# Kernel tuning notes

Hardware: AMD Instinct MI355X
Metric: run time of the kernel (lower is better)

The kernel has to match this reference:

```python
import jax, jax.numpy as jnp
import numpy as np

B, C, X, Y, Z = 2, 4, 128, 128, 96
_BIG = 1e10  # effectively infinite squared distance (no background in line)


def _edt_sq_pass(f, axis):
    """One separable pass of the exact squared EDT along `axis`:
    g[i] = min_j f[j] + (i - j)^2  (Felzenszwalb lower envelope, brute-forced
    with lax.map so only O(rest) memory per step)."""
    f = jnp.moveaxis(f, axis, -1)  # (..., L)
    idx = jnp.arange(f.shape[-1], dtype=f.dtype)
    g = jax.lax.map(lambda i: jnp.min(f + (i - idx) ** 2, axis=-1), idx)  # (L, ...)
    return jnp.moveaxis(jnp.moveaxis(g, 0, -1), -1, axis)


def _edt(mask):
    """Exact Euclidean distance of True voxels to the nearest False voxel
    (matches scipy.ndimage.distance_transform_edt on a binary mask)."""
    f = jnp.where(mask, _BIG, 0.0).astype(jnp.float32)
    for ax in (-3, -2, -1):  # three spatial axes
        f = _edt_sq_pass(f, ax)
    return jnp.sqrt(f)


def _neighbor(m, axis, d):
    """Shift `m` by d along `axis` with edge replication (reflect border,
    as in skimage's grey erosion used by find_boundaries)."""
    axis = axis % m.ndim
    pw = [(1, 1) if i == axis else (0, 0) for i in range(m.ndim)]
    p = jnp.pad(m, pw, mode='edge')
    sl = [slice(None)] * m.ndim
    sl[axis] = slice(1 + d, p.shape[axis] - 1 + d)
    return p[tuple(sl)]


def _inner_boundary(m):
    """skimage find_boundaries(mode='inner', connectivity=1): foreground voxels
    with at least one background face-neighbor."""
    eroded = m
    for ax in (-3, -2, -1):
        eroded = eroded & _neighbor(m, ax, 1) & _neighbor(m, ax, -1)
    return m & ~eroded


def _compute_sdf(onehot):
    """Signed distance map per (batch, class): negdis - posdis, zero on the
    inner boundary; zero where the class is absent; channel 0 is skipped."""
    posdis = _edt(onehot)          # dist inside object to background
    negdis = _edt(~onehot)         # dist outside object to foreground
    sdf = jnp.where(_inner_boundary(onehot), 0.0, negdis - posdis)
    any_pos = jnp.any(onehot, axis=(2, 3, 4), keepdims=True)
    sdf = jnp.where(any_pos, sdf, 0.0)
    return sdf.at[:, 0].set(0.0)   # loop starts at c=1 in the original


def setup_inputs() -> dict:
    key = jax.random.key(0)
    k1, k2 = jax.random.split(key)
    net_output = jax.random.normal(k1, (B, C, X, Y, Z), dtype=jnp.float32)
    gt = jax.random.randint(k2, (B, 1, X, Y, Z), 0, C, dtype=jnp.int32)
    return {"net_output": net_output, "gt": gt}


def reference(net_output, gt):
    probs = jax.nn.softmax(net_output, axis=1)  # softmax_helper = softmax over class dim
    classes = jnp.arange(net_output.shape[1], dtype=gt.dtype).reshape(1, -1, 1, 1, 1)
    onehot = gt == classes  # scatter_(1, gt, 1) one-hot, bool (B,C,X,Y,Z)
    phi = _compute_sdf(onehot)
    # einsum('bcxyz,bcxyz->bcxyz') on foreground channels, then global mean
    return jnp.mean(probs[:, 1:] * phi[:, 1:])
```

## Files before the change

kernel.cpp:

```cpp
#include <hip/hip_runtime.h>
#include <hip/hip_fp16.h>
#include <math.h>

#define XD 128
#define YD 128
#define ZD 96
#define NV (XD*YD*ZD)
#define SXX (YD*ZD)
#define SENT 49152
#define TW2 114
#define TDW (TW2/2)
#define TROWS 144
#define SCANB 192
#define PROBB 1024

__global__ __launch_bounds__(384) void k_scan_prob(const int* __restrict__ gt,
                                                   const float* __restrict__ net,
                                                   unsigned char* __restrict__ out,
                                                   __half2* __restrict__ probs,
                                                   int* __restrict__ flags,
                                                   int batch0) {
    const int bb  = blockIdx.y;
    const int myb = batch0 + bb;
    const int tid = threadIdx.x;

    if (blockIdx.x >= SCANB) {
        const int p = (blockIdx.x - SCANB) * 384 + tid;
        const int idx = p * 4;
        const float* nb = net + (size_t)myb * 4 * NV;
        float4 v0 = *(const float4*)(nb + idx);
        float4 v1 = *(const float4*)(nb + NV + idx);
        float4 v2 = *(const float4*)(nb + 2 * NV + idx);
        float4 v3 = *(const float4*)(nb + 3 * NV + idx);

        const float a0[4] = {v0.x, v0.y, v0.z, v0.w};
        const float a1[4] = {v1.x, v1.y, v1.z, v1.w};
        const float a2[4] = {v2.x, v2.y, v2.z, v2.w};
        const float a3[4] = {v3.x, v3.y, v3.z, v3.w};
        float p1[4], p2[4], p3[4];
#pragma unroll
        for (int j = 0; j < 4; ++j) {
            float mx = fmaxf(fmaxf(a0[j], a1[j]), fmaxf(a2[j], a3[j]));
            float e0 = __expf(a0[j] - mx);
            float e1 = __expf(a1[j] - mx);
            float e2 = __expf(a2[j] - mx);
            float e3 = __expf(a3[j] - mx);
            float iv = __frcp_rn(e0 + e1 + e2 + e3);
            p1[j] = e1 * iv; p2[j] = e2 * iv; p3[j] = e3 * iv;
        }
        __half2 h10 = __floats2half2_rn(p1[0], p1[1]);
        __half2 h11 = __floats2half2_rn(p1[2], p1[3]);
        __half2 h20 = __floats2half2_rn(p2[0], p2[1]);
        __half2 h21 = __floats2half2_rn(p2[2], p2[3]);
        __half2 h30 = __floats2half2_rn(p3[0], p3[1]);
        __half2 h31 = __floats2half2_rn(p3[2], p3[3]);
        ((__half2*)probs)[(size_t)(myb * 3 + 0) * (NV / 2) + 2 * p]     = h10;
        ((__half2*)probs)[(size_t)(myb * 3 + 0) * (NV / 2) + 2 * p + 1] = h11;
        ((__half2*)probs)[(size_t)(myb * 3 + 1) * (NV / 2) + 2 * p]     = h20;
        ((__half2*)probs)[(size_t)(myb * 3 + 1) * (NV / 2) + 2 * p + 1] = h21;
        ((__half2*)probs)[(size_t)(myb * 3 + 2) * (NV / 2) + 2 * p]     = h30;
        ((__half2*)probs)[(size_t)(myb * 3 + 2) * (NV / 2) + 2 * p + 1] = h31;
        return;
    }

    const int l   = tid & 63;
    const int w6  = tid >> 6;
    const int lq0 = blockIdx.x * 64;

    __shared__ unsigned char gtile[64 * 132];
    __shared__ int blkbits;
    if (tid == 0) blkbits = 0;

    int mybits = 0;
    const int* gp = gt + (size_t)myb * NV + lq0 + l;
    for (int j = w6; j < XD; j += 6) {
        int g = gp[(size_t)j * SXX];
        mybits |= 1 << g;
        gtile[l * 132 + j] = (unsigned char)g;
    }
#pragma unroll
    for (int off = 32; off; off >>= 1) mybits |= __shfl_xor(mybits, off);
    __syncthreads();
    if ((tid & 63) == 0) atomicOr(&blkbits, mybits);

    unsigned int D[32];
    {
        const unsigned int ci = (unsigned int)((w6 >> 1) + 1);
        const int s = w6 & 1;
        unsigned int G[32];
        const unsigned int* grow = (const unsigned int*)gtile + l * 33;
#pragma unroll
        for (int q = 0; q < 32; ++q) G[q] = grow[q];

        int cnt = 200;
#pragma unroll
        for (int q = 0; q < 32; ++q) {
            unsigned int u = G[q], dv = 0;
#pragma unroll
            for (int b = 0; b < 4; ++b) {
                unsigned int gv = (u >> (8 * b)) & 255u;
                bool zero = s ? (gv == ci) : (gv != ci);
                cnt = zero ? 0 : ((cnt < 200) ? cnt + 1 : 200);
                dv |= (unsigned int)cnt << (8 * b);
            }
            D[q] = dv;
        }
        cnt = 200;
#pragma unroll
        for (int q = 31; q >= 0; --q) {
            unsigned int u = G[q], dv = D[q];
#pragma unroll
            for (int b = 3; b >= 0; --b) {
                unsigned int gv = (u >> (8 * b)) & 255u;
                bool zero = s ? (gv == ci) : (gv != ci);
                cnt = zero ? 0 : ((cnt < 200) ? cnt + 1 : 200);
                unsigned int old = (dv >> (8 * b)) & 255u;
                unsigned int nbv = ((unsigned int)cnt < old) ? (unsigned int)cnt : old;
                dv = (dv & ~(255u << (8 * b))) | (nbv << (8 * b));
            }
            D[q] = dv;
        }
    }
    __syncthreads();
    if (tid == 0) atomicOr(&flags[myb], blkbits);

    {
        const int r = l & 3;
        unsigned char* ob = out + (size_t)(bb * 6 + w6) * NV + lq0 + (l & ~3);
#pragma unroll
        for (int q = 0; q < 32; ++q) {
            unsigned int A = D[q];
            unsigned int Bv = (unsigned int)__shfl_xor((int)A, 1);
            unsigned int t = (r & 1)
                ? __builtin_amdgcn_perm(A, Bv, 0x07030501u)
                : __builtin_amdgcn_perm(A, Bv, 0x02060004u);
            unsigned int Cv = (unsigned int)__shfl_xor((int)t, 2);
            unsigned int y = (r & 2)
                ? __builtin_amdgcn_perm(t, Cv, 0x07060302u)
                : __builtin_amdgcn_perm(t, Cv, 0x01000504u);
            *(unsigned int*)(ob + (size_t)(4 * q + r) * SXX) = y;
        }
    }
}

__device__ __forceinline__ bool edt_fast(const float r[32], float m[16]) {
#pragma unroll
    for (int k = 0; k < 16; ++k) m[k] = r[k + 8];
#pragma unroll
    for (int t = 1; t <= 4; ++t) {
        const float t2 = (float)(t * t);
#pragma unroll
        for (int k = 0; k < 16; ++k)
            m[k] = fminf(m[k], fminf(r[k + 8 - t], r[k + 8 + t]) + t2);
    }
    float mm = m[0];
#pragma unroll
    for (int k = 1; k < 16; ++k) mm = fmaxf(mm, m[k]);
    if (__all(mm <= 16.0f)) return true;
#pragma unroll
    for (int t = 5; t <= 8; ++t) {
        const float t2 = (float)(t * t);
#pragma unroll
        for (int k = 0; k < 16; ++k)
            m[k] = fminf(m[k], fminf(r[k + 8 - t], r[k + 8 + t]) + t2);
    }
    mm = m[0];
#pragma unroll
    for (int k = 1; k < 16; ++k) mm = fmaxf(mm, m[k]);
    return __all(mm <= 64.0f) != 0;
}

template<int STRIDE, int L>
__device__ __forceinline__ void edt_slow(const unsigned short* __restrict__ p0,
                                         int i0, float m[16]) {
    int t = 9;
    bool done = false;
    while (!done && t < L) {
        for (int u = 0; u < 4; ++u, ++t) {
            float t2 = (float)(t * t);
#pragma unroll
            for (int k = 0; k < 16; ++k) {
                int jm = i0 + k - t; if (jm < -8) jm = -8;
                int jp = i0 + k + t; if (jp > L + 7) jp = L + 7;
                m[k] = fminf(m[k], fminf((float)p0[jm * STRIDE],
                                         (float)p0[jp * STRIDE]) + t2);
            }
        }
        float mm = m[0];
#pragma unroll
        for (int k = 1; k < 16; ++k) mm = fmaxf(mm, m[k]);
        done = __all(mm <= (float)((t - 1) * (t - 1))) != 0;
    }
}

__global__ __launch_bounds__(768) void k_yz_acc(const unsigned char* __restrict__ in,
                                                const __half2* __restrict__ probs,
                                                const int* __restrict__ flags,
                                                double* __restrict__ partials,
                                                int batch0) {
    const int x   = blockIdx.x;
    const int bbl = blockIdx.y / 3;
    const int c   = blockIdx.y % 3;
    const int b   = batch0 + bbl;
    const int tid = threadIdx.x;
    const int pidx = (b * 3 + c) * XD + x;

    __shared__ unsigned short tile[TROWS * TW2];
    __shared__ double sd[768];
    unsigned int* t32 = (unsigned int*)tile;

    if (((flags[b] >> (c + 1)) & 1) == 0) {
        if (tid == 0) partials[pidx] = 0.0;
        return;
    }

    for (int i = tid; i < 16 * TDW; i += 768) {
        int r = i / TDW, cc = i - r * TDW;
        int row = (r < 8) ? r : 128 + r;
        t32[row * TDW + cc] = 0xFFFFFFFFu;
    }
    for (int i = tid; i < 128 * 9; i += 768) {
        int r = i / 9, cc = i - r * 9;
        int col = (cc < 4) ? cc : (48 + cc);
        t32[(8 + r) * TDW + col] = 0xFFFFFFFFu;
    }

    const int z0 = tid % 96;  const int iY = (tid / 96) * 16;
    const int y0 = tid % 128; const int iZ = (tid / 128) * 16;
    const int e  = tid * 16;
    const int sy = e / ZD, sz = e - sy * ZD;
    const unsigned int sbase = (8 + sy) * TDW + (8 + sz) / 2;

    float m[16];
    unsigned int dpp[8];

    {
        const uint4* ip = (const uint4*)(in + (size_t)(bbl * 6 + 2 * c) * NV +
                                         (size_t)x * SXX);
        uint4 v = ip[tid];
        unsigned int vv[4] = {v.x, v.y, v.z, v.w};
#pragma unroll
        for (int q = 0; q < 4; ++q) {
            unsigned int b0 = vv[q] & 255u, b1 = (vv[q] >> 8) & 255u;
            unsigned int b2 = (vv[q] >> 16) & 255u, b3 = vv[q] >> 24;
            t32[sbase + 2 * q] = (b0 > 127u ? SENT : b0 * b0) |
                                 ((b1 > 127u ? SENT : b1 * b1) << 16);
            t32[sbase + 2 * q + 1] = (b2 > 127u ? SENT : b2 * b2) |
                                     ((b3 > 127u ? SENT : b3 * b3) << 16);
        }
    }
    __syncthreads();
    {
        float r[32];
#pragma unroll
        for (int w = 0; w < 32; ++w) r[w] = (float)tile[(iY + w) * TW2 + 8 + z0];
        if (!edt_fast(r, m)) edt_slow<TW2, YD>(&tile[8 * TW2 + 8 + z0], iY, m);
        __syncthreads();
#pragma unroll
        for (int k = 0; k < 16; ++k)
            tile[(8 + iY + k) * TW2 + 8 + z0] =
                (unsigned short)fminf(m[k], (float)SENT);
        __syncthreads();
    }
    {
        float r[32];
        const unsigned int* wp = &t32[(8 + y0) * TDW + iZ / 2];
#pragma unroll
        for (int q = 0; q < 16; ++q) {
            unsigned int u = wp[q];
            r[2 * q] = (float)(u & 0xFFFFu);
            r[2 * q + 1] = (float)(u >> 16);
        }
        if (!edt_fast(r, m)) edt_slow<1, ZD>(&tile[(8 + y0) * TW2 + 8], iZ, m);
    }
#pragma unroll
    for (int q = 0; q < 8; ++q)
        dpp[q] = (unsigned int)fminf(m[2 * q], (float)SENT) |
                 ((unsigned int)fminf(m[2 * q + 1], (float)SENT) << 16);
    __syncthreads();

    {
        const uint4* ip = (const uint4*)(in + (size_t)(bbl * 6 + 2 * c + 1) * NV +
                                         (size_t)x * SXX);
        uint4 v = ip[tid];
        unsigned int vv[4] = {v.x, v.y, v.z, v.w};
#pragma unroll
        for (int q = 0; q < 4; ++q) {
            unsigned int b0 = vv[q] & 255u, b1 = (vv[q] >> 8) & 255u;
            unsigned int b2 = (vv[q] >> 16) & 255u, b3 = vv[q] >> 24;
            t32[sbase + 2 * q] = (b0 > 127u ? SENT : b0 * b0) |
                                 ((b1 > 127u ? SENT : b1 * b1) << 16);
            t32[sbase + 2 * q + 1] = (b2 > 127u ? SENT : b2 * b2) |
                                     ((b3 > 127u ? SENT : b3 * b3) << 16);
        }
    }
    __syncthreads();
    {
        float r[32];
#pragma unroll
        for (int w = 0; w < 32; ++w) r[w] = (float)tile[(iY + w) * TW2 + 8 + z0];
        if (!edt_fast(r, m)) edt_slow<TW2, YD>(&tile[8 * TW2 + 8 + z0], iY, m);
        __syncthreads();
#pragma unroll
        for (int k = 0; k < 16; ++k)
            tile[(8 + iY + k) * TW2 + 8 + z0] =
                (unsigned short)fminf(m[k], (float)SENT);
        __syncthreads();
    }
    {
        float r[32];
        const unsigned int* wp = &t32[(8 + y0) * TDW + iZ / 2];
#pragma unroll
        for (int q = 0; q < 16; ++q) {
            unsigned int u = wp[q];
            r[2 * q] = (float)(u & 0xFFFFu);
            r[2 * q + 1] = (float)(u >> 16);
        }
        if (!edt_fast(r, m)) edt_slow<1, ZD>(&tile[(8 + y0) * TW2 + 8], iZ, m);
    }

    float a = 0.0f;
    {
        const __half2* pv = probs + (size_t)(b * 3 + c) * (NV / 2) +
                            ((size_t)x * SXX + (size_t)y0 * ZD + iZ) / 2;
#pragma unroll
        for (int q = 0; q < 8; ++q) {
            float2 pf = __half22float2(pv[q]);
            unsigned int dp0 = dpp[q] & 0xFFFFu, dp1 = dpp[q] >> 16;
            float phi0 = (dp0 == 1u) ? 0.0f
                       : (sqrtf(m[2 * q]) - sqrtf((float)dp0));
            float phi1 = (dp1 == 1u) ? 0.0f
                       : (sqrtf(m[2 * q + 1]) - sqrtf((float)dp1));
            a += pf.x * phi0 + pf.y * phi1;
        }
    }
    sd[tid] = (double)a;
    __syncthreads();
    for (int off = 512; off; off >>= 1) {
        if (tid < off && tid + off < 768) sd[tid] += sd[tid + off];
        __syncthreads();
    }
    if (tid == 0) partials[pidx] = sd[0];
}

__global__ void k_reduce(const double* __restrict__ partials, int n,
                         float* __restrict__ out) {
    __shared__ double sd[256];
    double ls = 0.0;
    for (int i = threadIdx.x; i < n; i += 256) ls += partials[i];
    sd[threadIdx.x] = ls;
    __syncthreads();
    for (int off = 128; off > 0; off >>= 1) {
        if (threadIdx.x < off) sd[threadIdx.x] += sd[threadIdx.x + off];
        __syncthreads();
    }
    if (threadIdx.x == 0) out[0] = (float)(sd[0] / 9437184.0);
}

extern "C" void kernel_launch(void* const* d_in, const int* in_sizes, int n_in,
                              void* d_out, int out_size, void* d_ws, size_t ws_size,
                              hipStream_t stream) {
    const float* net = (const float*)d_in[0];
    const int*   gt  = (const int*)d_in[1];
    float* out = (float*)d_out;
    char* ws = (char*)d_ws;

    const size_t xbufB1  = (size_t)6 * NV;
    const size_t probsB  = (size_t)2 * 3 * NV * 2;
    const size_t tail    = (size_t)768 * sizeof(double) + 64;

    const int nb = (ws_size >= 2 * xbufB1 + probsB + tail) ? 2 : 1;

    unsigned char* xbuf  = (unsigned char*)ws;
    __half2*       probs = (__half2*)(ws + (size_t)nb * xbufB1);
    double*     partials = (double*)(ws + (size_t)nb * xbufB1 + probsB);
    int*           flags = (int*)((char*)partials + 768 * sizeof(double));

    hipMemsetAsync(flags, 0, 8 * sizeof(int), stream);

    for (int b0 = 0; b0 < 2; b0 += nb) {
        hipLaunchKernelGGL(k_scan_prob, dim3(SCANB + PROBB, nb), dim3(384), 0,
                           stream, gt, net, xbuf, probs, flags, b0);
        hipLaunchKernelGGL(k_yz_acc, dim3(XD, 3 * nb), dim3(768), 0, stream,
                           xbuf, probs, flags, partials, b0);
    }
    hipLaunchKernelGGL(k_reduce, dim3(1), dim3(256), 0, stream, partials,
                       768, out);
}
```

Before: 75.35 us.

## Run Y/Z EDT passes with packed u16 min/add instead of float

The Y and Z distance-transform passes in k_yz_acc now keep squared distances as packed 16-bit pairs and use v_pk_min_u16/v_pk_add_u16. This halves the ALU instruction count and register footprint compared with per-element float min/add. The thread mapping changes so that each thread handles 8 packed words, column-pair in Y and a 16-element chunk in Z, with alignbit used for the odd shifts. The rare long-distance fallback still runs in float. Risks are u16 saturation, since values are capped at the 49152 sentinel plus t² up to 64, and the added pack/unpack overhead on the slow path.

```diff
diff --git a/kernel.cpp b/kernel.cpp
--- a/kernel.cpp
+++ b/kernel.cpp
@@ -8,6 +8,7 @@
 #define NV (XD*YD*ZD)
 #define SXX (YD*ZD)
 #define SENT 49152
+#define SENTP 0xC000C000u
 #define TW2 114
 #define TDW (TW2/2)
 #define TROWS 144
@@ -48,18 +49,12 @@
             float iv = __frcp_rn(e0 + e1 + e2 + e3);
             p1[j] = e1 * iv; p2[j] = e2 * iv; p3[j] = e3 * iv;
         }
-        __half2 h10 = __floats2half2_rn(p1[0], p1[1]);
-        __half2 h11 = __floats2half2_rn(p1[2], p1[3]);
-        __half2 h20 = __floats2half2_rn(p2[0], p2[1]);
-        __half2 h21 = __floats2half2_rn(p2[2], p2[3]);
-        __half2 h30 = __floats2half2_rn(p3[0], p3[1]);
-        __half2 h31 = __floats2half2_rn(p3[2], p3[3]);
-        ((__half2*)probs)[(size_t)(myb * 3 + 0) * (NV / 2) + 2 * p]     = h10;
-        ((__half2*)probs)[(size_t)(myb * 3 + 0) * (NV / 2) + 2 * p + 1] = h11;
-        ((__half2*)probs)[(size_t)(myb * 3 + 1) * (NV / 2) + 2 * p]     = h20;
-        ((__half2*)probs)[(size_t)(myb * 3 + 1) * (NV / 2) + 2 * p + 1] = h21;
-        ((__half2*)probs)[(size_t)(myb * 3 + 2) * (NV / 2) + 2 * p]     = h30;
-        ((__half2*)probs)[(size_t)(myb * 3 + 2) * (NV / 2) + 2 * p + 1] = h31;
+        probs[(size_t)(myb * 3 + 0) * (NV / 2) + 2 * p]     = __floats2half2_rn(p1[0], p1[1]);
+        probs[(size_t)(myb * 3 + 0) * (NV / 2) + 2 * p + 1] = __floats2half2_rn(p1[2], p1[3]);
+        probs[(size_t)(myb * 3 + 1) * (NV / 2) + 2 * p]     = __floats2half2_rn(p2[0], p2[1]);
+        probs[(size_t)(myb * 3 + 1) * (NV / 2) + 2 * p + 1] = __floats2half2_rn(p2[2], p2[3]);
+        probs[(size_t)(myb * 3 + 2) * (NV / 2) + 2 * p]     = __floats2half2_rn(p3[0], p3[1]);
+        probs[(size_t)(myb * 3 + 2) * (NV / 2) + 2 * p + 1] = __floats2half2_rn(p3[2], p3[3]);
         return;
     }
 
@@ -143,42 +138,62 @@
     }
 }
 
-__device__ __forceinline__ bool edt_fast(const float r[32], float m[16]) {
-#pragma unroll
-    for (int k = 0; k < 16; ++k) m[k] = r[k + 8];
-#pragma unroll
-    for (int t = 1; t <= 4; ++t) {
-        const float t2 = (float)(t * t);
-#pragma unroll
-        for (int k = 0; k < 16; ++k)
-            m[k] = fminf(m[k], fminf(r[k + 8 - t], r[k + 8 + t]) + t2);
-    }
-    float mm = m[0];
-#pragma unroll
-    for (int k = 1; k < 16; ++k) mm = fmaxf(mm, m[k]);
-    if (__all(mm <= 16.0f)) return true;
-#pragma unroll
-    for (int t = 5; t <= 8; ++t) {
-        const float t2 = (float)(t * t);
-#pragma unroll
-        for (int k = 0; k < 16; ++k)
-            m[k] = fminf(m[k], fminf(r[k + 8 - t], r[k + 8 + t]) + t2);
-    }
-    mm = m[0];
-#pragma unroll
-    for (int k = 1; k < 16; ++k) mm = fmaxf(mm, m[k]);
-    return __all(mm <= 64.0f) != 0;
+__device__ __forceinline__ unsigned int pk_min(unsigned int a, unsigned int b) {
+    unsigned int d;
+    asm("v_pk_min_u16 %0, %1, %2" : "=v"(d) : "v"(a), "v"(b));
+    return d;
+}
+__device__ __forceinline__ unsigned int pk_max(unsigned int a, unsigned int b) {
+    unsigned int d;
+    asm("v_pk_max_u16 %0, %1, %2" : "=v"(d) : "v"(a), "v"(b));
+    return d;
+}
+__device__ __forceinline__ unsigned int pk_add(unsigned int a, unsigned int b) {
+    unsigned int d;
+    asm("v_pk_add_u16 %0, %1, %2" : "=v"(d) : "v"(a), "v"(b));
+    return d;
+}
+
+__device__ __forceinline__ bool pk_done(const unsigned int m[8], int thr) {
+    unsigned int mx = m[0];
+#pragma unroll
+    for (int k = 1; k < 8; ++k) mx = pk_max(mx, m[k]);
+    int a = (int)(mx & 0xFFFFu), bq = (int)(mx >> 16);
+    int amax = a > bq ? a : bq;
+    return __all(amax <= thr) != 0;
 }
 
 template<int STRIDE, int L>
-__device__ __forceinline__ void edt_slow(const unsigned short* __restrict__ p0,
-                                         int i0, float m[16]) {
+__device__ __forceinline__ void edt_slow8(const unsigned short* __restrict__ p0,
+                                          int i0, float m[8]) {
     int t = 9;
     bool done = false;
     while (!done && t < L) {
         for (int u = 0; u < 4; ++u, ++t) {
             float t2 = (float)(t * t);
 #pragma unroll
+            for (int k = 0; k < 8; ++k) {
+                int jm = i0 + k - t; if (jm < -8) jm = -8;
+                int jp = i0 + k + t; if (jp > L + 7) jp = L + 7;
+                m[k] = fminf(m[k], fminf((float)p0[jm * STRIDE],
+                                         (float)p0[jp * STRIDE]) + t2);
+            }
+        }
+        float mm = m[0];
+#pragma unroll
+        for (int k = 1; k < 8; ++k) mm = fmaxf(mm, m[k]);
+        done = __all(mm <= (float)((t - 1) * (t - 1))) != 0;
+    }
+}
+template<int STRIDE, int L>
+__device__ __forceinline__ void edt_slow16(const unsigned short* __restrict__ p0,
+                                           int i0, float m[16]) {
+    int t = 9;
+    bool done = false;
+    while (!done && t < L) {
+        for (int u = 0; u < 4; ++u, ++t) {
+            float t2 = (float)(t * t);
+#pragma unroll
             for (int k = 0; k < 16; ++k) {
                 int jm = i0 + k - t; if (jm < -8) jm = -8;
                 int jp = i0 + k + t; if (jp > L + 7) jp = L + 7;
@@ -190,6 +205,114 @@
 #pragma unroll
         for (int k = 1; k < 16; ++k) mm = fmaxf(mm, m[k]);
         done = __all(mm <= (float)((t - 1) * (t - 1))) != 0;
+    }
+}
+
+__device__ __forceinline__ void edtY_pk(unsigned int* __restrict__ t32,
+                                        unsigned short* __restrict__ tile,
+                                        int zp, int i0, unsigned int m[8]) {
+    unsigned int w[24];
+    unsigned int* colp = t32 + 4 + zp;
+#pragma unroll
+    for (int q = 0; q < 24; ++q) w[q] = colp[(i0 + q) * TDW];
+#pragma unroll
+    for (int k = 0; k < 8; ++k) m[k] = w[k + 8];
+#pragma unroll
+    for (int t = 1; t <= 4; ++t) {
+        const unsigned int t2p = (unsigned int)(t * t) * 0x00010001u;
+#pragma unroll
+        for (int k = 0; k < 8; ++k)
+            m[k] = pk_min(m[k], pk_add(pk_min(w[k + 8 - t], w[k + 8 + t]), t2p));
+    }
+    bool done = pk_done(m, 16);
+    if (!done) {
+#pragma unroll
+        for (int t = 5; t <= 8; ++t) {
+            const unsigned int t2p = (unsigned int)(t * t) * 0x00010001u;
+#pragma unroll
+            for (int k = 0; k < 8; ++k)
+                m[k] = pk_min(m[k], pk_add(pk_min(w[k + 8 - t], w[k + 8 + t]), t2p));
+        }
+        done = pk_done(m, 64);
+    }
+    if (!done) {
+#pragma unroll
+        for (int h = 0; h < 2; ++h) {
+            float fm[8];
+#pragma unroll
+            for (int k = 0; k < 8; ++k)
+                fm[k] = (float)(h ? (m[k] >> 16) : (m[k] & 0xFFFFu));
+            edt_slow8<TW2, YD>(&tile[8 * TW2 + 8 + 2 * zp + h], i0, fm);
+#pragma unroll
+            for (int k = 0; k < 8; ++k) {
+                unsigned int v = (unsigned int)fm[k];
+                m[k] = h ? ((m[k] & 0x0000FFFFu) | (v << 16))
+                         : ((m[k] & 0xFFFF0000u) | v);
+            }
+        }
+    }
+#pragma unroll
+    for (int k = 0; k < 8; ++k) m[k] = pk_min(m[k], SENTP);
+}
+
+__device__ __forceinline__ void edtZ_pk(const unsigned int* __restrict__ t32,
+                                        const unsigned short* __restrict__ tile,
+                                        int y0, int ch, unsigned int m[8]) {
+    unsigned int w[16];
+    const unsigned int* rowp = t32 + (size_t)(8 + y0) * TDW;
+#pragma unroll
+    for (int q = 0; q < 16; ++q) w[q] = rowp[8 * ch + q];
+#pragma unroll
+    for (int k = 0; k < 8; ++k) m[k] = w[k + 4];
+#pragma unroll
+    for (int t = 1; t <= 4; ++t) {
+        const unsigned int t2p = (unsigned int)(t * t) * 0x00010001u;
+#pragma unroll
+        for (int k = 0; k < 8; ++k) {
+            unsigned int lo, hi;
+            if (t & 1) {
+                lo = __builtin_amdgcn_alignbit(w[k + 4 - (t - 1) / 2],
+                                               w[k + 4 - (t + 1) / 2], 16);
+                hi = __builtin_amdgcn_alignbit(w[k + 4 + (t + 1) / 2],
+                                               w[k + 4 + (t - 1) / 2], 16);
+            } else {
+                lo = w[k + 4 - t / 2]; hi = w[k + 4 + t / 2];
+            }
+            m[k] = pk_min(m[k], pk_add(pk_min(lo, hi), t2p));
+        }
+    }
+    bool done = pk_done(m, 16);
+    if (!done) {
+#pragma unroll
+        for (int t = 5; t <= 8; ++t) {
+            const unsigned int t2p = (unsigned int)(t * t) * 0x00010001u;
+#pragma unroll
+            for (int k = 0; k < 8; ++k) {
+                unsigned int lo, hi;
+                if (t & 1) {
+                    lo = __builtin_amdgcn_alignbit(w[k + 4 - (t - 1) / 2],
+                                                   w[k + 4 - (t + 1) / 2], 16);
+                    hi = __builtin_amdgcn_alignbit(w[k + 4 + (t + 1) / 2],
+                                                   w[k + 4 + (t - 1) / 2], 16);
+                } else {
+                    lo = w[k + 4 - t / 2]; hi = w[k + 4 + t / 2];
+                }
+                m[k] = pk_min(m[k], pk_add(pk_min(lo, hi), t2p));
+            }
+        }
+        done = pk_done(m, 64);
+    }
+    if (!done) {
+        float fm[16];
+#pragma unroll
+        for (int k = 0; k < 8; ++k) {
+            fm[2 * k]     = (float)(m[k] & 0xFFFFu);
+            fm[2 * k + 1] = (float)(m[k] >> 16);
+        }
+        edt_slow16<1, ZD>(&tile[(8 + y0) * TW2 + 8], 16 * ch, fm);
+#pragma unroll
+        for (int k = 0; k < 8; ++k)
+            m[k] = (unsigned int)fm[2 * k] | ((unsigned int)fm[2 * k + 1] << 16);
     }
 }
 
@@ -217,22 +340,21 @@
     for (int i = tid; i < 16 * TDW; i += 768) {
         int r = i / TDW, cc = i - r * TDW;
         int row = (r < 8) ? r : 128 + r;
-        t32[row * TDW + cc] = 0xFFFFFFFFu;
+        t32[row * TDW + cc] = SENTP;
     }
     for (int i = tid; i < 128 * 9; i += 768) {
         int r = i / 9, cc = i - r * 9;
         int col = (cc < 4) ? cc : (48 + cc);
-        t32[(8 + r) * TDW + col] = 0xFFFFFFFFu;
-    }
-
-    const int z0 = tid % 96;  const int iY = (tid / 96) * 16;
-    const int y0 = tid % 128; const int iZ = (tid / 128) * 16;
+        t32[(8 + r) * TDW + col] = SENTP;
+    }
+
+    const int zp = tid % 48;  const int iY = (tid / 48) * 8;
+    const int y0 = tid % 128; const int ch = tid / 128;
     const int e  = tid * 16;
     const int sy = e / ZD, sz = e - sy * ZD;
     const unsigned int sbase = (8 + sy) * TDW + (8 + sz) / 2;
 
-    float m[16];
-    unsigned int dpp[8];
+    unsigned int m[8], dpp[8];
 
     {
         const uint4* ip = (const uint4*)(in + (size_t)(bbl * 6 + 2 * c) * NV +
@@ -250,33 +372,17 @@
         }
     }
     __syncthreads();
-    {
-        float r[32];
-#pragma unroll
-        for (int w = 0; w < 32; ++w) r[w] = (float)tile[(iY + w) * TW2 + 8 + z0];
-        if (!edt_fast(r, m)) edt_slow<TW2, YD>(&tile[8 * TW2 + 8 + z0], iY, m);
-        __syncthreads();
-#pragma unroll
-        for (int k = 0; k < 16; ++k)
-            tile[(8 + iY + k) * TW2 + 8 + z0] =
-                (unsigned short)fminf(m[k], (float)SENT);
-        __syncthreads();
-    }
-    {
-        float r[32];
-        const unsigned int* wp = &t32[(8 + y0) * TDW + iZ / 2];
-#pragma unroll
-        for (int q = 0; q < 16; ++q) {
-            unsigned int u = wp[q];
-            r[2 * q] = (float)(u & 0xFFFFu);
-            r[2 * q + 1] = (float)(u >> 16);
-        }
-        if (!edt_fast(r, m)) edt_slow<1, ZD>(&tile[(8 + y0) * TW2 + 8], iZ, m);
-    }
-#pragma unroll
-    for (int q = 0; q < 8; ++q)
-        dpp[q] = (unsigned int)fminf(m[2 * q], (float)SENT) |
-                 ((unsigned int)fminf(m[2 * q + 1], (float)SENT) << 16);
+    edtY_pk(t32, tile, zp, iY, m);
+    __syncthreads();
+    {
+        unsigned int* colp = t32 + 4 + zp;
+#pragma unroll
+        for (int k = 0; k < 8; ++k) colp[(iY + k + 8) * TDW] = m[k];
+    }
+    __syncthreads();
+    edtZ_pk(t32, tile, y0, ch, m);
+#pragma unroll
+    for (int q = 0; q < 8; ++q) dpp[q] = pk_min(m[q], SENTP);
     __syncthreads();
 
     {
@@ -295,42 +401,30 @@
         }
     }
     __syncthreads();
-    {
-        float r[32];
-#pragma unroll
-        for (int w = 0; w < 32; ++w) r[w] = (float)tile[(iY + w) * TW2 + 8 + z0];
-        if (!edt_fast(r, m)) edt_slow<TW2, YD>(&tile[8 * TW2 + 8 + z0], iY, m);
-        __syncthreads();
-#pragma unroll
-        for (int k = 0; k < 16; ++k)
-            tile[(8 + iY + k) * TW2 + 8 + z0] =
-                (unsigned short)fminf(m[k], (float)SENT);
-        __syncthreads();
-    }
-    {
-        float r[32];
-        const unsigned int* wp = &t32[(8 + y0) * TDW + iZ / 2];
-#pragma unroll
-        for (int q = 0; q < 16; ++q) {
-            unsigned int u = wp[q];
-            r[2 * q] = (float)(u & 0xFFFFu);
-            r[2 * q + 1] = (float)(u >> 16);
-        }
-        if (!edt_fast(r, m)) edt_slow<1, ZD>(&tile[(8 + y0) * TW2 + 8], iZ, m);
-    }
+    edtY_pk(t32, tile, zp, iY, m);
+    __syncthreads();
+    {
+        unsigned int* colp = t32 + 4 + zp;
+#pragma unroll
+        for (int k = 0; k < 8; ++k) colp[(iY + k + 8) * TDW] = m[k];
+    }
+    __syncthreads();
+    edtZ_pk(t32, tile, y0, ch, m);
 
     float a = 0.0f;
     {
         const __half2* pv = probs + (size_t)(b * 3 + c) * (NV / 2) +
-                            ((size_t)x * SXX + (size_t)y0 * ZD + iZ) / 2;
+                            ((size_t)x * SXX + (size_t)y0 * ZD + 16 * ch) / 2;
 #pragma unroll
         for (int q = 0; q < 8; ++q) {
             float2 pf = __half22float2(pv[q]);
+            unsigned int dnq = pk_min(m[q], SENTP);
             unsigned int dp0 = dpp[q] & 0xFFFFu, dp1 = dpp[q] >> 16;
+            unsigned int dn0 = dnq & 0xFFFFu,   dn1 = dnq >> 16;
             float phi0 = (dp0 == 1u) ? 0.0f
-                       : (sqrtf(m[2 * q]) - sqrtf((float)dp0));
+                       : (sqrtf((float)dn0) - sqrtf((float)dp0));
             float phi1 = (dp1 == 1u) ? 0.0f
-                       : (sqrtf(m[2 * q + 1]) - sqrtf((float)dp1));
+                       : (sqrtf((float)dn1) - sqrtf((float)dp1));
             a += pf.x * phi0 + pf.y * phi1;
         }
     }
@@ -365,15 +459,15 @@
     float* out = (float*)d_out;
     char* ws = (char*)d_ws;
 
-    const size_t xbufB1  = (size_t)6 * NV;
-    const size_t probsB  = (size_t)2 * 3 * NV * 2;
-    const size_t tail    = (size_t)768 * sizeof(double) + 64;
+    const size_t xbufB1 = (size_t)6 * NV;
+    const size_t probsB = (size_t)2 * 3 * NV * 2;
+    const size_t tail   = (size_t)768 * sizeof(double) + 64;
 
     const int nb = (ws_size >= 2 * xbufB1 + probsB + tail) ? 2 : 1;
 
     unsigned char* xbuf  = (unsigned char*)ws;
     __half2*       probs = (__half2*)(ws + (size_t)nb * xbufB1);
-    double*     partials = (double*)(ws + (size_t)nb * xbufB1 + probsB);
+    double*     partials = (double*)((char*)probs + probsB);
     int*           flags = (int*)((char*)partials + 768 * sizeof(double));
 
     hipMemsetAsync(flags, 0, 8 * sizeof(int), stream);
```

New measurement: 69.99 us. 1.08x faster.
